# Kernel tuning notes

Measured on AMD Instinct MI355X. Metric: run time of the kernel, lower is better.

## Reference

```python
import jax, jax.numpy as jnp
import numpy as np

EPS = 1e-10


def spmm(rows, cols, vals, x, n_rows):
    # COO sparse [n_rows, *] @ dense x : out[r] = sum_e vals[e] * x[cols[e]]
    return jax.ops.segment_sum(vals[:, None] * x[cols], rows, num_segments=n_rows)


def setup_inputs() -> dict:
    key = jax.random.key(0)
    ks = jax.random.split(key, 16)
    n_in, n_full, n_nodes, d, nnz, n_out = 65536, 65536, 131072, 256, 262144, 16384
    return {
        "mu": jax.random.normal(ks[0], (n_in, d), jnp.float32),
        "var": jax.random.uniform(ks[1], (n_in, d), jnp.float32),
        "mu_history": jax.random.normal(ks[2], (n_nodes, d), jnp.float32),
        "var_history": jax.random.uniform(ks[3], (n_nodes, d), jnp.float32),
        "adj_vals": jax.random.uniform(ks[4], (nnz,), jnp.float32),
        "fadj_vals": jax.random.uniform(ks[5], (nnz,), jnp.float32),
        "madj_vals": jax.random.uniform(ks[6], (nnz,), jnp.float32),
        "adj_rows": jax.random.randint(ks[7], (nnz,), 0, n_out, jnp.int32),
        "adj_cols": jax.random.randint(ks[8], (nnz,), 0, n_in, jnp.int32),
        "fadj_rows": jax.random.randint(ks[9], (nnz,), 0, n_out, jnp.int32),
        "fadj_cols": jax.random.randint(ks[10], (nnz,), 0, n_full, jnp.int32),
        "madj_rows": jax.random.randint(ks[11], (nnz,), 0, n_out, jnp.int32),
        "madj_cols": jax.random.randint(ks[12], (nnz,), 0, n_in, jnp.int32),
        "ifield": jax.random.randint(ks[13], (n_in,), 0, n_nodes, jnp.int32),
        "ffield": jax.random.randint(ks[14], (n_full,), 0, n_nodes, jnp.int32),
        "n_out": n_out,
    }


def reference(mu, var, mu_history, var_history,
              adj_vals, fadj_vals, madj_vals,
              adj_rows, adj_cols, fadj_rows, fadj_cols, madj_rows, madj_cols,
              ifield, ffield, n_out):
    # VRAggregator._call, tuple-(mu, var) branch, normalization != 'gcn'
    mu_self = mu[:n_out]
    var_self = var[:n_out]
    delta_mu = mu - mu_history[ifield]          # [n_in, d]
    mu_bar = mu_history[ffield]                 # [n_full, d]
    sigma = jnp.sqrt(var)
    sigma_bar = jnp.sqrt(var_history[ifield])
    delta_sigma = sigma - sigma_bar
    var_bar = var_history[ffield]
    msigma = delta_sigma * sigma_bar
    mu_neighbour = (spmm(adj_rows, adj_cols, adj_vals, delta_mu, n_out)
                    + spmm(fadj_rows, fadj_cols, fadj_vals, mu_bar, n_out))
    var_neighbour = (spmm(adj_rows, adj_cols, adj_vals * adj_vals, delta_sigma * delta_sigma, n_out)
                     + spmm(fadj_rows, fadj_cols, fadj_vals * fadj_vals, var_bar, n_out)
                     + 2.0 * spmm(madj_rows, madj_cols, madj_vals, msigma, n_out))
    var_neighbour = jax.nn.relu(var_neighbour) + EPS
    return (jnp.concatenate((mu_self, mu_neighbour), axis=1),
            jnp.concatenate((var_self, var_neighbour), axis=1))
```

## Files before the change

### kernel.cpp

```cpp
#include <hip/hip_runtime.h>

#define EPS_F 1e-10f

typedef unsigned int u32;

__device__ __forceinline__ u32 bf16pair(float lo, float hi) {
  u32 a = __float_as_uint(lo);
  u32 b = __float_as_uint(hi);
  a = a + 0x7FFFu + ((a >> 16) & 1u);
  b = b + 0x7FFFu + ((b >> 16) & 1u);
  return (a >> 16) | (b & 0xFFFF0000u);
}
__device__ __forceinline__ float bf_lo(u32 u) { return __uint_as_float(u << 16); }
__device__ __forceinline__ float bf_hi(u32 u) { return __uint_as_float(u & 0xFFFF0000u); }

__global__ __launch_bounds__(256) void k_count3(
    const int* __restrict__ ra, const int* __restrict__ rf,
    const int* __restrict__ rm, int* __restrict__ cnt, int nnz, int n_out) {
  int total = 3 * nnz;
  for (int i = blockIdx.x * blockDim.x + threadIdx.x; i < total;
       i += gridDim.x * blockDim.x) {
    int m = (i >= nnz) + (i >= 2 * nnz);
    int e = i - m * nnz;
    const int* rp = (m == 0) ? ra : (m == 1) ? rf : rm;
    atomicAdd(&cnt[m * n_out + rp[e]], 1);
  }
}

__global__ __launch_bounds__(256) void k_scan3(const int* __restrict__ cnt_all,
                                               int* __restrict__ base_all,
                                               int* __restrict__ cur_all, int n) {
  const int* cnt = cnt_all + blockIdx.x * n;
  int* base = base_all + blockIdx.x * (n + 1);
  int* cur = cur_all + blockIdx.x * n;
  __shared__ int sums[256];
  int tid = threadIdx.x;
  int chunk = (n + 255) / 256;
  int s = tid * chunk, e = min(s + chunk, n);
  int local = 0;
  for (int i = s; i < e; ++i) local += cnt[i];
  sums[tid] = local;
  __syncthreads();
  for (int off = 1; off < 256; off <<= 1) {
    int v = (tid >= off) ? sums[tid - off] : 0;
    __syncthreads();
    sums[tid] += v;
    __syncthreads();
  }
  int run = (tid == 0) ? 0 : sums[tid - 1];
  for (int i = s; i < e; ++i) {
    base[i] = run;
    cur[i] = run;
    run += cnt[i];
  }
  if (tid == 255) base[n] = sums[255];
}

__global__ __launch_bounds__(256) void k_scatter3(
    const int* __restrict__ ra, const int* __restrict__ ca, const float* __restrict__ va,
    const int* __restrict__ rf, const int* __restrict__ cf, const float* __restrict__ vf,
    const int* __restrict__ rm, const int* __restrict__ cm, const float* __restrict__ vm,
    const int* __restrict__ ffield,
    int* __restrict__ cur_all, uint2* __restrict__ ord, int nnz, int n_out) {
  int total = 3 * nnz;
  for (int i = blockIdx.x * blockDim.x + threadIdx.x; i < total;
       i += gridDim.x * blockDim.x) {
    int m = (i >= nnz) + (i >= 2 * nnz);
    int e = i - m * nnz;
    const int* rp = (m == 0) ? ra : (m == 1) ? rf : rm;
    const int* cp = (m == 0) ? ca : (m == 1) ? cf : cm;
    const float* vp = (m == 0) ? va : (m == 1) ? vf : vm;
    int r = rp[e];
    int c = cp[e];
    float w = vp[e];
    if (m == 1) c = ffield[c];
    if (m == 2) w = 2.0f * w;
    int pos = atomicAdd(&cur_all[m * n_out + r], 1);
    ord[(size_t)m * nnz + pos] = make_uint2((u32)c, __float_as_uint(w));
  }
}

__global__ __launch_bounds__(256) void k_pre(
    const float* __restrict__ mu, const float* __restrict__ var,
    const float* __restrict__ muh, const float* __restrict__ varh,
    const int* __restrict__ ifield,
    u32* __restrict__ A, u32* __restrict__ M, int n_in) {
  int wave = (int)((blockIdx.x * blockDim.x + threadIdx.x) >> 6);
  int lane = threadIdx.x & 63;
  int nw = (int)((gridDim.x * blockDim.x) >> 6);
  for (int row = wave; row < n_in; row += nw) {
    int f = ifield[row];
    float4 m  = ((const float4*)(mu   + (size_t)row * 256))[lane];
    float4 v  = ((const float4*)(var  + (size_t)row * 256))[lane];
    float4 mh = ((const float4*)(muh  + (size_t)f   * 256))[lane];
    float4 vh = ((const float4*)(varh + (size_t)f   * 256))[lane];
    float4 d, q, p;
    float s, sb, ds;
    s = sqrtf(v.x); sb = sqrtf(vh.x); ds = s - sb; d.x = m.x - mh.x; q.x = ds * ds; p.x = ds * sb;
    s = sqrtf(v.y); sb = sqrtf(vh.y); ds = s - sb; d.y = m.y - mh.y; q.y = ds * ds; p.y = ds * sb;
    s = sqrtf(v.z); sb = sqrtf(vh.z); ds = s - sb; d.z = m.z - mh.z; q.z = ds * ds; p.z = ds * sb;
    s = sqrtf(v.w); sb = sqrtf(vh.w); ds = s - sb; d.w = m.w - mh.w; q.w = ds * ds; p.w = ds * sb;
    uint4 au;
    au.x = bf16pair(d.x, d.y);
    au.y = bf16pair(d.z, d.w);
    au.z = bf16pair(q.x, q.y);
    au.w = bf16pair(q.z, q.w);
    ((uint4*)(A + (size_t)row * 256))[lane] = au;
    uint2 mu2;
    mu2.x = bf16pair(p.x, p.y);
    mu2.y = bf16pair(p.z, p.w);
    ((uint2*)(M + (size_t)row * 128))[lane] = mu2;
  }
}

__global__ __launch_bounds__(256) void k_agg(
    const float* __restrict__ mu, const float* __restrict__ var,
    const float* __restrict__ muh, const float* __restrict__ varh,
    const u32* __restrict__ A, const u32* __restrict__ M,
    const int* __restrict__ base_all, const uint2* __restrict__ ord,
    float* __restrict__ out0, float* __restrict__ out1, int n_out, int nnz) {
  int r = (int)((blockIdx.x * blockDim.x + threadIdx.x) >> 6);
  int lane = threadIdx.x & 63;
  if (r >= n_out) return;

  float4 am = make_float4(0.f, 0.f, 0.f, 0.f);
  float4 av = make_float4(0.f, 0.f, 0.f, 0.f);

  {
    const int* base = base_all;
    const uint2* o = ord;
    int b0 = base[r], b1 = base[r + 1];
    int p = b0;
    for (; p + 1 < b1; p += 2) {
      uint2 cv0 = o[p], cv1 = o[p + 1];
      float w0 = __uint_as_float(cv0.y), w1 = __uint_as_float(cv1.y);
      uint4 u0 = ((const uint4*)(A + (size_t)cv0.x * 256))[lane];
      uint4 u1 = ((const uint4*)(A + (size_t)cv1.x * 256))[lane];
      float q0 = w0 * w0, q1 = w1 * w1;
      am.x += w0 * bf_lo(u0.x) + w1 * bf_lo(u1.x);
      am.y += w0 * bf_hi(u0.x) + w1 * bf_hi(u1.x);
      am.z += w0 * bf_lo(u0.y) + w1 * bf_lo(u1.y);
      am.w += w0 * bf_hi(u0.y) + w1 * bf_hi(u1.y);
      av.x += q0 * bf_lo(u0.z) + q1 * bf_lo(u1.z);
      av.y += q0 * bf_hi(u0.z) + q1 * bf_hi(u1.z);
      av.z += q0 * bf_lo(u0.w) + q1 * bf_lo(u1.w);
      av.w += q0 * bf_hi(u0.w) + q1 * bf_hi(u1.w);
    }
    if (p < b1) {
      uint2 cv0 = o[p];
      float w0 = __uint_as_float(cv0.y);
      uint4 u0 = ((const uint4*)(A + (size_t)cv0.x * 256))[lane];
      float q0 = w0 * w0;
      am.x += w0 * bf_lo(u0.x); am.y += w0 * bf_hi(u0.x);
      am.z += w0 * bf_lo(u0.y); am.w += w0 * bf_hi(u0.y);
      av.x += q0 * bf_lo(u0.z); av.y += q0 * bf_hi(u0.z);
      av.z += q0 * bf_lo(u0.w); av.w += q0 * bf_hi(u0.w);
    }
  }

  {
    const int* base = base_all + (n_out + 1);
    const uint2* o = ord + (size_t)nnz;
    int b0 = base[r], b1 = base[r + 1];
    int p = b0;
    for (; p + 1 < b1; p += 2) {
      uint2 cv0 = o[p], cv1 = o[p + 1];
      float w0 = __uint_as_float(cv0.y), w1 = __uint_as_float(cv1.y);
      float4 m0 = ((const float4*)(muh  + (size_t)cv0.x * 256))[lane];
      float4 v0 = ((const float4*)(varh + (size_t)cv0.x * 256))[lane];
      float4 m1 = ((const float4*)(muh  + (size_t)cv1.x * 256))[lane];
      float4 v1 = ((const float4*)(varh + (size_t)cv1.x * 256))[lane];
      float q0 = w0 * w0, q1 = w1 * w1;
      am.x += w0 * m0.x + w1 * m1.x; am.y += w0 * m0.y + w1 * m1.y;
      am.z += w0 * m0.z + w1 * m1.z; am.w += w0 * m0.w + w1 * m1.w;
      av.x += q0 * v0.x + q1 * v1.x; av.y += q0 * v0.y + q1 * v1.y;
      av.z += q0 * v0.z + q1 * v1.z; av.w += q0 * v0.w + q1 * v1.w;
    }
    if (p < b1) {
      uint2 cv0 = o[p];
      float w0 = __uint_as_float(cv0.y);
      float4 m0 = ((const float4*)(muh  + (size_t)cv0.x * 256))[lane];
      float4 v0 = ((const float4*)(varh + (size_t)cv0.x * 256))[lane];
      float q0 = w0 * w0;
      am.x += w0 * m0.x; am.y += w0 * m0.y; am.z += w0 * m0.z; am.w += w0 * m0.w;
      av.x += q0 * v0.x; av.y += q0 * v0.y; av.z += q0 * v0.z; av.w += q0 * v0.w;
    }
  }

  {
    const int* base = base_all + 2 * (n_out + 1);
    const uint2* o = ord + 2 * (size_t)nnz;
    int b0 = base[r], b1 = base[r + 1];
    int p = b0;
    for (; p + 1 < b1; p += 2) {
      uint2 cv0 = o[p], cv1 = o[p + 1];
      float w0 = __uint_as_float(cv0.y), w1 = __uint_as_float(cv1.y);
      uint2 x0 = ((const uint2*)(M + (size_t)cv0.x * 128))[lane];
      uint2 x1 = ((const uint2*)(M + (size_t)cv1.x * 128))[lane];
      av.x += w0 * bf_lo(x0.x) + w1 * bf_lo(x1.x);
      av.y += w0 * bf_hi(x0.x) + w1 * bf_hi(x1.x);
      av.z += w0 * bf_lo(x0.y) + w1 * bf_lo(x1.y);
      av.w += w0 * bf_hi(x0.y) + w1 * bf_hi(x1.y);
    }
    if (p < b1) {
      uint2 cv0 = o[p];
      float w0 = __uint_as_float(cv0.y);
      uint2 x0 = ((const uint2*)(M + (size_t)cv0.x * 128))[lane];
      av.x += w0 * bf_lo(x0.x); av.y += w0 * bf_hi(x0.x);
      av.z += w0 * bf_lo(x0.y); av.w += w0 * bf_hi(x0.y);
    }
  }

  av.x = fmaxf(av.x, 0.f) + EPS_F;
  av.y = fmaxf(av.y, 0.f) + EPS_F;
  av.z = fmaxf(av.z, 0.f) + EPS_F;
  av.w = fmaxf(av.w, 0.f) + EPS_F;
  float4 msf = ((const float4*)(mu  + (size_t)r * 256))[lane];
  float4 vsf = ((const float4*)(var + (size_t)r * 256))[lane];
  ((float4*)(out0 + (size_t)r * 512))[lane]       = msf;
  ((float4*)(out0 + (size_t)r * 512 + 256))[lane] = am;
  ((float4*)(out1 + (size_t)r * 512))[lane]       = vsf;
  ((float4*)(out1 + (size_t)r * 512 + 256))[lane] = av;
}

__global__ __launch_bounds__(256) void k_init_out(
    const float* __restrict__ mu, const float* __restrict__ var,
    float* __restrict__ out0, float* __restrict__ out1) {
  int r = blockIdx.x;
  int t = threadIdx.x;
  const float4 z = make_float4(0.f, 0.f, 0.f, 0.f);
  if (t < 128) {
    float4* dst = (float4*)(out0 + (size_t)r * 512);
    dst[t] = (t < 64) ? ((const float4*)(mu + (size_t)r * 256))[t] : z;
  } else {
    int u = t - 128;
    float4* dst = (float4*)(out1 + (size_t)r * 512);
    dst[u] = (u < 64) ? ((const float4*)(var + (size_t)r * 256))[u] : z;
  }
}

__global__ __launch_bounds__(256) void k_edge_adj_fb(
    const float* __restrict__ vals, const int* __restrict__ rows,
    const int* __restrict__ cols,
    const float* __restrict__ mu, const float* __restrict__ var,
    const float* __restrict__ muh, const float* __restrict__ varh,
    const int* __restrict__ ifield,
    float* __restrict__ out0, float* __restrict__ out1, int nnz) {
  int wave = (int)((blockIdx.x * blockDim.x + threadIdx.x) >> 6);
  int lane = threadIdx.x & 63;
  int nw = (int)((gridDim.x * blockDim.x) >> 6);
  for (int e = wave; e < nnz; e += nw) {
    float w = vals[e];
    int r = rows[e];
    int c = cols[e];
    int f = ifield[c];
    float4 m  = ((const float4*)(mu   + (size_t)c * 256))[lane];
    float4 v  = ((const float4*)(var  + (size_t)c * 256))[lane];
    float4 mh = ((const float4*)(muh  + (size_t)f * 256))[lane];
    float4 vh = ((const float4*)(varh + (size_t)f * 256))[lane];
    float4 xm, xv;
    float ds;
    xm.x = m.x - mh.x; ds = sqrtf(v.x) - sqrtf(vh.x); xv.x = ds * ds;
    xm.y = m.y - mh.y; ds = sqrtf(v.y) - sqrtf(vh.y); xv.y = ds * ds;
    xm.z = m.z - mh.z; ds = sqrtf(v.z) - sqrtf(vh.z); xv.z = ds * ds;
    xm.w = m.w - mh.w; ds = sqrtf(v.w) - sqrtf(vh.w); xv.w = ds * ds;
    float w2 = w * w;
    float* om = out0 + (size_t)r * 512 + 256 + lane * 4;
    float* ov = out1 + (size_t)r * 512 + 256 + lane * 4;
    atomicAdd(om + 0, w * xm.x); atomicAdd(om + 1, w * xm.y);
    atomicAdd(om + 2, w * xm.z); atomicAdd(om + 3, w * xm.w);
    atomicAdd(ov + 0, w2 * xv.x); atomicAdd(ov + 1, w2 * xv.y);
    atomicAdd(ov + 2, w2 * xv.z); atomicAdd(ov + 3, w2 * xv.w);
  }
}

__global__ __launch_bounds__(256) void k_edge_fadj_fb(
    const float* __restrict__ vals, const int* __restrict__ rows,
    const int* __restrict__ cols,
    const float* __restrict__ muh, const float* __restrict__ varh,
    const int* __restrict__ ffield,
    float* __restrict__ out0, float* __restrict__ out1, int nnz) {
  int wave = (int)((blockIdx.x * blockDim.x + threadIdx.x) >> 6);
  int lane = threadIdx.x & 63;
  int nw = (int)((gridDim.x * blockDim.x) >> 6);
  for (int e = wave; e < nnz; e += nw) {
    float w = vals[e];
    int r = rows[e];
    int f = ffield[cols[e]];
    float4 mb = ((const float4*)(muh  + (size_t)f * 256))[lane];
    float4 vb = ((const float4*)(varh + (size_t)f * 256))[lane];
    float w2 = w * w;
    float* om = out0 + (size_t)r * 512 + 256 + lane * 4;
    float* ov = out1 + (size_t)r * 512 + 256 + lane * 4;
    atomicAdd(om + 0, w * mb.x); atomicAdd(om + 1, w * mb.y);
    atomicAdd(om + 2, w * mb.z); atomicAdd(om + 3, w * mb.w);
    atomicAdd(ov + 0, w2 * vb.x); atomicAdd(ov + 1, w2 * vb.y);
    atomicAdd(ov + 2, w2 * vb.z); atomicAdd(ov + 3, w2 * vb.w);
  }
}

__global__ __launch_bounds__(256) void k_edge_madj_fb(
    const float* __restrict__ vals, const int* __restrict__ rows,
    const int* __restrict__ cols,
    const float* __restrict__ var, const float* __restrict__ varh,
    const int* __restrict__ ifield,
    float* __restrict__ out1, int nnz) {
  int wave = (int)((blockIdx.x * blockDim.x + threadIdx.x) >> 6);
  int lane = threadIdx.x & 63;
  int nw = (int)((gridDim.x * blockDim.x) >> 6);
  for (int e = wave; e < nnz; e += nw) {
    float w = 2.0f * vals[e];
    int r = rows[e];
    int c = cols[e];
    int f = ifield[c];
    float4 v  = ((const float4*)(var  + (size_t)c * 256))[lane];
    float4 vh = ((const float4*)(varh + (size_t)f * 256))[lane];
    float4 x;
    float sb;
    sb = sqrtf(vh.x); x.x = (sqrtf(v.x) - sb) * sb;
    sb = sqrtf(vh.y); x.y = (sqrtf(v.y) - sb) * sb;
    sb = sqrtf(vh.z); x.z = (sqrtf(v.z) - sb) * sb;
    sb = sqrtf(vh.w); x.w = (sqrtf(v.w) - sb) * sb;
    float* ov = out1 + (size_t)r * 512 + 256 + lane * 4;
    atomicAdd(ov + 0, w * x.x); atomicAdd(ov + 1, w * x.y);
    atomicAdd(ov + 2, w * x.z); atomicAdd(ov + 3, w * x.w);
  }
}

__global__ __launch_bounds__(256) void k_final(float* __restrict__ out1, int n_out) {
  int total = n_out * 64;
  for (int i = blockIdx.x * blockDim.x + threadIdx.x; i < total;
       i += gridDim.x * blockDim.x) {
    int r = i >> 6;
    int q = i & 63;
    float4* p = (float4*)(out1 + (size_t)r * 512 + 256) + q;
    float4 v = *p;
    v.x = fmaxf(v.x, 0.f) + EPS_F;
    v.y = fmaxf(v.y, 0.f) + EPS_F;
    v.z = fmaxf(v.z, 0.f) + EPS_F;
    v.w = fmaxf(v.w, 0.f) + EPS_F;
    *p = v;
  }
}

extern "C" void kernel_launch(void* const* d_in, const int* in_sizes, int n_in_args,
                              void* d_out, int out_size, void* d_ws, size_t ws_size,
                              hipStream_t stream) {
  const float* mu        = (const float*)d_in[0];
  const float* var       = (const float*)d_in[1];
  const float* muh       = (const float*)d_in[2];
  const float* varh      = (const float*)d_in[3];
  const float* adj_vals  = (const float*)d_in[4];
  const float* fadj_vals = (const float*)d_in[5];
  const float* madj_vals = (const float*)d_in[6];
  const int* adj_rows    = (const int*)d_in[7];
  const int* adj_cols    = (const int*)d_in[8];
  const int* fadj_rows   = (const int*)d_in[9];
  const int* fadj_cols   = (const int*)d_in[10];
  const int* madj_rows   = (const int*)d_in[11];
  const int* madj_cols   = (const int*)d_in[12];
  const int* ifield      = (const int*)d_in[13];
  const int* ffield      = (const int*)d_in[14];

  const int n_out = out_size / 1024;
  const int n_in  = in_sizes[0] / 256;
  const int nnz   = in_sizes[4];

  float* out0 = (float*)d_out;
  float* out1 = out0 + (size_t)n_out * 512;

  const size_t uA = (size_t)n_in * 256;
  const size_t uM = (size_t)n_in * 128;
  const size_t uOrd = (size_t)3 * nnz * 2;
  const size_t uCnt = (size_t)3 * n_out;
  const size_t uBase = (size_t)3 * (n_out + 1);
  const size_t need = (uA + uM + uOrd + uCnt + uBase + uCnt) * sizeof(u32);

  if (ws_size >= need) {
    u32* A = (u32*)d_ws;
    u32* M = A + uA;
    uint2* ord = (uint2*)(M + uM);
    int* cnt  = (int*)(M + uM + uOrd);
    int* base = cnt + uCnt;
    int* cur  = base + uBase;

    hipMemsetAsync(cnt, 0, uCnt * sizeof(int), stream);
    k_count3<<<1024, 256, 0, stream>>>(adj_rows, fadj_rows, madj_rows, cnt, nnz, n_out);
    k_scan3<<<3, 256, 0, stream>>>(cnt, base, cur, n_out);
    k_scatter3<<<1024, 256, 0, stream>>>(adj_rows, adj_cols, adj_vals,
                                         fadj_rows, fadj_cols, fadj_vals,
                                         madj_rows, madj_cols, madj_vals,
                                         ffield, cur, ord, nnz, n_out);
    k_pre<<<4096, 256, 0, stream>>>(mu, var, muh, varh, ifield, A, M, n_in);
    int blocks = (n_out * 64 + 255) / 256;
    k_agg<<<blocks, 256, 0, stream>>>(mu, var, muh, varh, A, M, base, ord,
                                      out0, out1, n_out, nnz);
  } else {
    k_init_out<<<n_out, 256, 0, stream>>>(mu, var, out0, out1);
    k_edge_adj_fb<<<4096, 256, 0, stream>>>(adj_vals, adj_rows, adj_cols,
                                            mu, var, muh, varh, ifield, out0, out1, nnz);
    k_edge_madj_fb<<<4096, 256, 0, stream>>>(madj_vals, madj_rows, madj_cols,
                                             var, varh, ifield, out1, nnz);
    k_edge_fadj_fb<<<4096, 256, 0, stream>>>(fadj_vals, fadj_rows, fadj_cols,
                                             muh, varh, ffield, out0, out1, nnz);
    k_final<<<4096, 256, 0, stream>>>(out1, n_out);
  }
}
```

Baseline: 324.8 us.

## Precompute bf16 packed ffield-gathered history table and fuse count into pre kernel

Adds a packed bf16 table FB holding mu_history and var_history gathered through ffield for every full node, built in the pre kernel, so the aggregation reads one 16-byte chunk per fadj edge instead of two fp32 float4 loads. The edge row-count pass is merged into the pre kernel, removing a launch. In exchange it writes an extra n_full×1KB table and converts history values to bf16, which loses precision. The whole path depends on the workspace being large enough.

```diff
diff --git a/kernel.cpp b/kernel.cpp
--- a/kernel.cpp
+++ b/kernel.cpp
@@ -14,16 +14,65 @@
 __device__ __forceinline__ float bf_lo(u32 u) { return __uint_as_float(u << 16); }
 __device__ __forceinline__ float bf_hi(u32 u) { return __uint_as_float(u & 0xFFFF0000u); }
 
-__global__ __launch_bounds__(256) void k_count3(
+template <bool WITH_FB>
+__global__ __launch_bounds__(256) void k_pre(
+    const float* __restrict__ mu, const float* __restrict__ var,
+    const float* __restrict__ muh, const float* __restrict__ varh,
+    const int* __restrict__ ifield, const int* __restrict__ ffield,
     const int* __restrict__ ra, const int* __restrict__ rf,
-    const int* __restrict__ rm, int* __restrict__ cnt, int nnz, int n_out) {
+    const int* __restrict__ rm, int* __restrict__ cnt,
+    u32* __restrict__ A, u32* __restrict__ M, u32* __restrict__ FB,
+    int n_in, int n_full, int n_out, int nnz) {
+  int tid = blockIdx.x * blockDim.x + threadIdx.x;
+  int nth = gridDim.x * blockDim.x;
+
   int total = 3 * nnz;
-  for (int i = blockIdx.x * blockDim.x + threadIdx.x; i < total;
-       i += gridDim.x * blockDim.x) {
+  for (int i = tid; i < total; i += nth) {
     int m = (i >= nnz) + (i >= 2 * nnz);
     int e = i - m * nnz;
     const int* rp = (m == 0) ? ra : (m == 1) ? rf : rm;
     atomicAdd(&cnt[m * n_out + rp[e]], 1);
+  }
+
+  int wave = tid >> 6;
+  int lane = tid & 63;
+  int nw = nth >> 6;
+  int nr = WITH_FB ? max(n_in, n_full) : n_in;
+  for (int row = wave; row < nr; row += nw) {
+    if (row < n_in) {
+      int f = ifield[row];
+      float4 m  = ((const float4*)(mu   + (size_t)row * 256))[lane];
+      float4 v  = ((const float4*)(var  + (size_t)row * 256))[lane];
+      float4 mh = ((const float4*)(muh  + (size_t)f   * 256))[lane];
+      float4 vh = ((const float4*)(varh + (size_t)f   * 256))[lane];
+      float4 d, q, p;
+      float s, sb, ds;
+      s = sqrtf(v.x); sb = sqrtf(vh.x); ds = s - sb; d.x = m.x - mh.x; q.x = ds * ds; p.x = ds * sb;
+      s = sqrtf(v.y); sb = sqrtf(vh.y); ds = s - sb; d.y = m.y - mh.y; q.y = ds * ds; p.y = ds * sb;
+      s = sqrtf(v.z); sb = sqrtf(vh.z); ds = s - sb; d.z = m.z - mh.z; q.z = ds * ds; p.z = ds * sb;
+      s = sqrtf(v.w); sb = sqrtf(vh.w); ds = s - sb; d.w = m.w - mh.w; q.w = ds * ds; p.w = ds * sb;
+      uint4 au;
+      au.x = bf16pair(d.x, d.y);
+      au.y = bf16pair(d.z, d.w);
+      au.z = bf16pair(q.x, q.y);
+      au.w = bf16pair(q.z, q.w);
+      ((uint4*)(A + (size_t)row * 256))[lane] = au;
+      uint2 mu2;
+      mu2.x = bf16pair(p.x, p.y);
+      mu2.y = bf16pair(p.z, p.w);
+      ((uint2*)(M + (size_t)row * 128))[lane] = mu2;
+    }
+    if (WITH_FB && row < n_full) {
+      int f = ffield[row];
+      float4 mb = ((const float4*)(muh  + (size_t)f * 256))[lane];
+      float4 vb = ((const float4*)(varh + (size_t)f * 256))[lane];
+      uint4 fu;
+      fu.x = bf16pair(mb.x, mb.y);
+      fu.y = bf16pair(mb.z, mb.w);
+      fu.z = bf16pair(vb.x, vb.y);
+      fu.w = bf16pair(vb.z, vb.w);
+      ((uint4*)(FB + (size_t)row * 256))[lane] = fu;
+    }
   }
 }
 
@@ -56,6 +105,7 @@
   if (tid == 255) base[n] = sums[255];
 }
 
+template <bool RESOLVE_F>
 __global__ __launch_bounds__(256) void k_scatter3(
     const int* __restrict__ ra, const int* __restrict__ ca, const float* __restrict__ va,
     const int* __restrict__ rf, const int* __restrict__ cf, const float* __restrict__ vf,
@@ -73,50 +123,19 @@
     int r = rp[e];
     int c = cp[e];
     float w = vp[e];
-    if (m == 1) c = ffield[c];
+    if (RESOLVE_F && m == 1) c = ffield[c];
     if (m == 2) w = 2.0f * w;
     int pos = atomicAdd(&cur_all[m * n_out + r], 1);
     ord[(size_t)m * nnz + pos] = make_uint2((u32)c, __float_as_uint(w));
   }
 }
 
-__global__ __launch_bounds__(256) void k_pre(
-    const float* __restrict__ mu, const float* __restrict__ var,
-    const float* __restrict__ muh, const float* __restrict__ varh,
-    const int* __restrict__ ifield,
-    u32* __restrict__ A, u32* __restrict__ M, int n_in) {
-  int wave = (int)((blockIdx.x * blockDim.x + threadIdx.x) >> 6);
-  int lane = threadIdx.x & 63;
-  int nw = (int)((gridDim.x * blockDim.x) >> 6);
-  for (int row = wave; row < n_in; row += nw) {
-    int f = ifield[row];
-    float4 m  = ((const float4*)(mu   + (size_t)row * 256))[lane];
-    float4 v  = ((const float4*)(var  + (size_t)row * 256))[lane];
-    float4 mh = ((const float4*)(muh  + (size_t)f   * 256))[lane];
-    float4 vh = ((const float4*)(varh + (size_t)f   * 256))[lane];
-    float4 d, q, p;
-    float s, sb, ds;
-    s = sqrtf(v.x); sb = sqrtf(vh.x); ds = s - sb; d.x = m.x - mh.x; q.x = ds * ds; p.x = ds * sb;
-    s = sqrtf(v.y); sb = sqrtf(vh.y); ds = s - sb; d.y = m.y - mh.y; q.y = ds * ds; p.y = ds * sb;
-    s = sqrtf(v.z); sb = sqrtf(vh.z); ds = s - sb; d.z = m.z - mh.z; q.z = ds * ds; p.z = ds * sb;
-    s = sqrtf(v.w); sb = sqrtf(vh.w); ds = s - sb; d.w = m.w - mh.w; q.w = ds * ds; p.w = ds * sb;
-    uint4 au;
-    au.x = bf16pair(d.x, d.y);
-    au.y = bf16pair(d.z, d.w);
-    au.z = bf16pair(q.x, q.y);
-    au.w = bf16pair(q.z, q.w);
-    ((uint4*)(A + (size_t)row * 256))[lane] = au;
-    uint2 mu2;
-    mu2.x = bf16pair(p.x, p.y);
-    mu2.y = bf16pair(p.z, p.w);
-    ((uint2*)(M + (size_t)row * 128))[lane] = mu2;
-  }
-}
-
+template <bool HAS_FB>
 __global__ __launch_bounds__(256) void k_agg(
     const float* __restrict__ mu, const float* __restrict__ var,
     const float* __restrict__ muh, const float* __restrict__ varh,
     const u32* __restrict__ A, const u32* __restrict__ M,
+    const u32* __restrict__ FB,
     const int* __restrict__ base_all, const uint2* __restrict__ ord,
     float* __restrict__ out0, float* __restrict__ out1, int n_out, int nnz) {
   int r = (int)((blockIdx.x * blockDim.x + threadIdx.x) >> 6);
@@ -163,27 +182,55 @@
     const uint2* o = ord + (size_t)nnz;
     int b0 = base[r], b1 = base[r + 1];
     int p = b0;
-    for (; p + 1 < b1; p += 2) {
-      uint2 cv0 = o[p], cv1 = o[p + 1];
-      float w0 = __uint_as_float(cv0.y), w1 = __uint_as_float(cv1.y);
-      float4 m0 = ((const float4*)(muh  + (size_t)cv0.x * 256))[lane];
-      float4 v0 = ((const float4*)(varh + (size_t)cv0.x * 256))[lane];
-      float4 m1 = ((const float4*)(muh  + (size_t)cv1.x * 256))[lane];
-      float4 v1 = ((const float4*)(varh + (size_t)cv1.x * 256))[lane];
-      float q0 = w0 * w0, q1 = w1 * w1;
-      am.x += w0 * m0.x + w1 * m1.x; am.y += w0 * m0.y + w1 * m1.y;
-      am.z += w0 * m0.z + w1 * m1.z; am.w += w0 * m0.w + w1 * m1.w;
-      av.x += q0 * v0.x + q1 * v1.x; av.y += q0 * v0.y + q1 * v1.y;
-      av.z += q0 * v0.z + q1 * v1.z; av.w += q0 * v0.w + q1 * v1.w;
-    }
-    if (p < b1) {
-      uint2 cv0 = o[p];
-      float w0 = __uint_as_float(cv0.y);
-      float4 m0 = ((const float4*)(muh  + (size_t)cv0.x * 256))[lane];
-      float4 v0 = ((const float4*)(varh + (size_t)cv0.x * 256))[lane];
-      float q0 = w0 * w0;
-      am.x += w0 * m0.x; am.y += w0 * m0.y; am.z += w0 * m0.z; am.w += w0 * m0.w;
-      av.x += q0 * v0.x; av.y += q0 * v0.y; av.z += q0 * v0.z; av.w += q0 * v0.w;
+    if (HAS_FB) {
+      for (; p + 1 < b1; p += 2) {
+        uint2 cv0 = o[p], cv1 = o[p + 1];
+        float w0 = __uint_as_float(cv0.y), w1 = __uint_as_float(cv1.y);
+        uint4 u0 = ((const uint4*)(FB + (size_t)cv0.x * 256))[lane];
+        uint4 u1 = ((const uint4*)(FB + (size_t)cv1.x * 256))[lane];
+        float q0 = w0 * w0, q1 = w1 * w1;
+        am.x += w0 * bf_lo(u0.x) + w1 * bf_lo(u1.x);
+        am.y += w0 * bf_hi(u0.x) + w1 * bf_hi(u1.x);
+        am.z += w0 * bf_lo(u0.y) + w1 * bf_lo(u1.y);
+        am.w += w0 * bf_hi(u0.y) + w1 * bf_hi(u1.y);
+        av.x += q0 * bf_lo(u0.z) + q1 * bf_lo(u1.z);
+        av.y += q0 * bf_hi(u0.z) + q1 * bf_hi(u1.z);
+        av.z += q0 * bf_lo(u0.w) + q1 * bf_lo(u1.w);
+        av.w += q0 * bf_hi(u0.w) + q1 * bf_hi(u1.w);
+      }
+      if (p < b1) {
+        uint2 cv0 = o[p];
+        float w0 = __uint_as_float(cv0.y);
+        uint4 u0 = ((const uint4*)(FB + (size_t)cv0.x * 256))[lane];
+        float q0 = w0 * w0;
+        am.x += w0 * bf_lo(u0.x); am.y += w0 * bf_hi(u0.x);
+        am.z += w0 * bf_lo(u0.y); am.w += w0 * bf_hi(u0.y);
+        av.x += q0 * bf_lo(u0.z); av.y += q0 * bf_hi(u0.z);
+        av.z += q0 * bf_lo(u0.w); av.w += q0 * bf_hi(u0.w);
+      }
+    } else {
+      for (; p + 1 < b1; p += 2) {
+        uint2 cv0 = o[p], cv1 = o[p + 1];
+        float w0 = __uint_as_float(cv0.y), w1 = __uint_as_float(cv1.y);
+        float4 m0 = ((const float4*)(muh  + (size_t)cv0.x * 256))[lane];
+        float4 v0 = ((const float4*)(varh + (size_t)cv0.x * 256))[lane];
+        float4 m1 = ((const float4*)(muh  + (size_t)cv1.x * 256))[lane];
+        float4 v1 = ((const float4*)(varh + (size_t)cv1.x * 256))[lane];
+        float q0 = w0 * w0, q1 = w1 * w1;
+        am.x += w0 * m0.x + w1 * m1.x; am.y += w0 * m0.y + w1 * m1.y;
+        am.z += w0 * m0.z + w1 * m1.z; am.w += w0 * m0.w + w1 * m1.w;
+        av.x += q0 * v0.x + q1 * v1.x; av.y += q0 * v0.y + q1 * v1.y;
+        av.z += q0 * v0.z + q1 * v1.z; av.w += q0 * v0.w + q1 * v1.w;
+      }
+      if (p < b1) {
+        uint2 cv0 = o[p];
+        float w0 = __uint_as_float(cv0.y);
+        float4 m0 = ((const float4*)(muh  + (size_t)cv0.x * 256))[lane];
+        float4 v0 = ((const float4*)(varh + (size_t)cv0.x * 256))[lane];
+        float q0 = w0 * w0;
+        am.x += w0 * m0.x; am.y += w0 * m0.y; am.z += w0 * m0.z; am.w += w0 * m0.w;
+        av.x += q0 * v0.x; av.y += q0 * v0.y; av.z += q0 * v0.z; av.w += q0 * v0.w;
+      }
     }
   }
 
@@ -362,39 +409,64 @@
   const int* ifield      = (const int*)d_in[13];
   const int* ffield      = (const int*)d_in[14];
 
-  const int n_out = out_size / 1024;
-  const int n_in  = in_sizes[0] / 256;
-  const int nnz   = in_sizes[4];
+  const int n_out  = out_size / 1024;
+  const int n_in   = in_sizes[0] / 256;
+  const int nnz    = in_sizes[4];
+  const int n_full = in_sizes[14];
 
   float* out0 = (float*)d_out;
   float* out1 = out0 + (size_t)n_out * 512;
 
   const size_t uA = (size_t)n_in * 256;
   const size_t uM = (size_t)n_in * 128;
+  const size_t uFB = (size_t)n_full * 256;
   const size_t uOrd = (size_t)3 * nnz * 2;
   const size_t uCnt = (size_t)3 * n_out;
   const size_t uBase = (size_t)3 * (n_out + 1);
-  const size_t need = (uA + uM + uOrd + uCnt + uBase + uCnt) * sizeof(u32);
-
-  if (ws_size >= need) {
+  const size_t need2 = (uA + uM + uOrd + uCnt + uBase + uCnt) * sizeof(u32);
+  const size_t need1 = need2 + uFB * sizeof(u32);
+
+  if (ws_size >= need2) {
+    const bool fb = (ws_size >= need1);
     u32* A = (u32*)d_ws;
     u32* M = A + uA;
-    uint2* ord = (uint2*)(M + uM);
-    int* cnt  = (int*)(M + uM + uOrd);
+    u32* FB = M + uM;
+    u32* tail = fb ? (FB + uFB) : (M + uM);
+    uint2* ord = (uint2*)tail;
+    int* cnt  = (int*)(tail + uOrd);
     int* base = cnt + uCnt;
     int* cur  = base + uBase;
 
     hipMemsetAsync(cnt, 0, uCnt * sizeof(int), stream);
-    k_count3<<<1024, 256, 0, stream>>>(adj_rows, fadj_rows, madj_rows, cnt, nnz, n_out);
+    if (fb) {
+      k_pre<true><<<4096, 256, 0, stream>>>(mu, var, muh, varh, ifield, ffield,
+                                            adj_rows, fadj_rows, madj_rows, cnt,
+                                            A, M, FB, n_in, n_full, n_out, nnz);
+    } else {
+      k_pre<false><<<4096, 256, 0, stream>>>(mu, var, muh, varh, ifield, ffield,
+                                             adj_rows, fadj_rows, madj_rows, cnt,
+                                             A, M, nullptr, n_in, n_full, n_out, nnz);
+    }
     k_scan3<<<3, 256, 0, stream>>>(cnt, base, cur, n_out);
-    k_scatter3<<<1024, 256, 0, stream>>>(adj_rows, adj_cols, adj_vals,
-                                         fadj_rows, fadj_cols, fadj_vals,
-                                         madj_rows, madj_cols, madj_vals,
-                                         ffield, cur, ord, nnz, n_out);
-    k_pre<<<4096, 256, 0, stream>>>(mu, var, muh, varh, ifield, A, M, n_in);
+    if (fb) {
+      k_scatter3<false><<<1024, 256, 0, stream>>>(adj_rows, adj_cols, adj_vals,
+                                                  fadj_rows, fadj_cols, fadj_vals,
+                                                  madj_rows, madj_cols, madj_vals,
+                                                  ffield, cur, ord, nnz, n_out);
+    } else {
+      k_scatter3<true><<<1024, 256, 0, stream>>>(adj_rows, adj_cols, adj_vals,
+                                                 fadj_rows, fadj_cols, fadj_vals,
+                                                 madj_rows, madj_cols, madj_vals,
+                                                 ffield, cur, ord, nnz, n_out);
+    }
     int blocks = (n_out * 64 + 255) / 256;
-    k_agg<<<blocks, 256, 0, stream>>>(mu, var, muh, varh, A, M, base, ord,
-                                      out0, out1, n_out, nnz);
+    if (fb) {
+      k_agg<true><<<blocks, 256, 0, stream>>>(mu, var, muh, varh, A, M, FB, base, ord,
+                                              out0, out1, n_out, nnz);
+    } else {
+      k_agg<false><<<blocks, 256, 0, stream>>>(mu, var, muh, varh, A, M, nullptr, base, ord,
+                                               out0, out1, n_out, nnz);
+    }
   } else {
     k_init_out<<<n_out, 256, 0, stream>>>(mu, var, out0, out1);
     k_edge_adj_fb<<<4096, 256, 0, stream>>>(adj_vals, adj_rows, adj_cols,
```

Measured after the change: 314.0 us. 1.03x faster.
